# Performance work log

Hardware: AMD Instinct MI355X
Metric: run time of the kernel (lower is better)

The kernel has to match this reference:

```python
import jax, jax.numpy as jnp
import numpy as np

NEG_SLOPE = 0.2

def sage_mean(src_h, dst_h, sidx, didx, n_dst, W_self, W_neigh, bias, edge_weight=None):
    # DGL SAGEConv 'mean': h = fc_self(dst) + fc_neigh(mean_{e in N(v)} src[e] * ew[e]) + bias
    m = src_h[sidx]                                   # [E, d] gather
    if edge_weight is not None:
        m = m * edge_weight[:, None]
    agg = jax.ops.segment_sum(m, didx, num_segments=n_dst)           # [n_dst, d]
    deg = jax.ops.segment_sum(jnp.ones((didx.shape[0],), m.dtype), didx, num_segments=n_dst)
    neigh = agg / jnp.maximum(deg, 1.0)[:, None]      # zero-degree nodes -> 0 (DGL behavior)
    return dst_h @ W_self.T + neigh @ W_neigh.T + bias


def setup_inputs() -> dict:
    key = jax.random.key(0)
    ks = jax.random.split(key, 20)
    n_k, n_e, d, E = 10000, 100000, 128, 1600000
    L = 2
    s = 0.05  # weight scale ~ xavier-ish
    inp = {
        'ii': jax.random.normal(ks[0], (n_k, d), jnp.float32),
        'e_emb': jax.random.normal(ks[1], (n_e, d), jnp.float32),
        'k_emb_weight': jax.random.normal(ks[2], (n_k, d), jnp.float32),
        'cf_ew': jax.random.uniform(ks[3], (E,), jnp.float32),
        'belong_src': jax.random.randint(ks[4], (E,), 0, n_k),
        'belong_dst': jax.random.randint(ks[5], (E,), 0, n_e),
        'collab_src': jax.random.randint(ks[6], (E,), 0, n_e),
        'collab_dst': jax.random.randint(ks[7], (E,), 0, n_e),
        'ek_self': jax.random.normal(ks[8], (L, d, d), jnp.float32) * s,
        'ek_neigh': jax.random.normal(ks[9], (L, d, d), jnp.float32) * s,
        'ek_bias': jnp.zeros((L, d), jnp.float32),
        'ee_self': jax.random.normal(ks[10], (L, d, d), jnp.float32) * s,
        'ee_neigh': jax.random.normal(ks[11], (L, d, d), jnp.float32) * s,
        'ee_bias': jnp.zeros((L, d), jnp.float32),
        'w1_W': jax.random.normal(ks[12], (d, 2 * d), jnp.float32) * s,
        'w1_b': jnp.zeros((d,), jnp.float32),
        'w2_W': jax.random.normal(ks[13], (d, d), jnp.float32) * s,
        'w2_b': jnp.zeros((d,), jnp.float32),
        'w3_W': jax.random.normal(ks[14], (d, d), jnp.float32) * s,
        'w3_b': jnp.zeros((d,), jnp.float32),
        'w4_W': jax.random.normal(ks[15], (d, 2 * d), jnp.float32) * s,
        'w4_b': jnp.zeros((d,), jnp.float32),
        'comb_W': jax.random.normal(ks[16], (d, 2 * d), jnp.float32) * s,
        'comb_b': jnp.zeros((d,), jnp.float32),
    }
    return inp


def reference(ii, e_emb, k_emb_weight, cf_ew, belong_src, belong_dst, collab_src, collab_dst,
              ek_self, ek_neigh, ek_bias, ee_self, ee_neigh, ee_bias,
              w1_W, w1_b, w2_W, w2_b, w3_W, w3_b, w4_W, w4_b, comb_W, comb_b):
    n_e = e_emb.shape[0]
    L = ek_self.shape[0]
    # ii = w4([ii ; k_emb.weight])
    ii2 = jnp.concatenate([ii, k_emb_weight], axis=1) @ w4_W.T + w4_b
    # knowledge -> employee SAGE stack ('belong')
    dst = e_emb
    for i in range(L - 1):
        dst = jax.nn.relu(sage_mean(ii2, dst, belong_src, belong_dst, n_e,
                                    ek_self[i], ek_neigh[i], ek_bias[i]))
    h_iI = sage_mean(ii2, dst, belong_src, belong_dst, n_e,
                     ek_self[L - 1], ek_neigh[L - 1], ek_bias[L - 1])
    h_iI = h_iI @ w2_W.T + w2_b
    # employee -> employee SAGE stack ('collaborate', edge-weighted)
    src_com = jnp.concatenate([h_iI, e_emb], axis=1) @ w1_W.T + w1_b
    dst = e_emb
    for i in range(L - 1):
        dst = jax.nn.relu(sage_mean(src_com, dst, collab_src, collab_dst, n_e,
                                    ee_self[i], ee_neigh[i], ee_bias[i], cf_ew))
    h_iS = sage_mean(src_com, dst, collab_src, collab_dst, n_e,
                     ee_self[L - 1], ee_neigh[L - 1], ee_bias[L - 1], cf_ew)
    h_iS = h_iS @ w3_W.T + w3_b
    h = jnp.concatenate([h_iI, h_iS], axis=1) @ comb_W.T + comb_b
    return jnp.where(h >= 0, h, NEG_SLOPE * h)  # LeakyReLU(0.2)
```

## Files before the change

kernel.cpp:

```cpp
#include <hip/hip_runtime.h>

#define D 128

using f16   = _Float16;
using f16x4 = __attribute__((ext_vector_type(4))) _Float16;
using f16x8 = __attribute__((ext_vector_type(8))) _Float16;
using f32x4 = __attribute__((ext_vector_type(4))) float;

__device__ __forceinline__ f16x8 zero8() {
    f16x8 v;
    #pragma unroll
    for (int j = 0; j < 8; ++j) v[j] = (f16)0;
    return v;
}

template<bool H>
__device__ __forceinline__ void stage_and_mfma(
    const void* Xv, const float* W, int ws,
    f16 (*sX)[136], f16 (*sW)[136],
    int tid, int row0, int M, int wave, int lm, int lg, f32x4 acc[8])
{
    __syncthreads();
    if (H) {
        const f16* X = (const f16*)Xv;
        #pragma unroll
        for (int i = 0; i < 4; ++i) {
            int idx = i * 256 + tid;
            int r   = idx >> 4;
            int kc  = idx & 15;
            f16x8 v = zero8();
            int gr = row0 + r;
            if (gr < M) v = *reinterpret_cast<const f16x8*>(X + (size_t)gr * D + kc * 8);
            *reinterpret_cast<f16x8*>(&sX[r][kc * 8]) = v;
        }
    } else {
        const float* X = (const float*)Xv;
        #pragma unroll
        for (int i = 0; i < 8; ++i) {
            int idx = i * 256 + tid;
            int r   = idx >> 5;
            int kq  = idx & 31;
            float4 v = make_float4(0.f, 0.f, 0.f, 0.f);
            int gr = row0 + r;
            if (gr < M) v = *reinterpret_cast<const float4*>(X + (size_t)gr * D + kq * 4);
            f16x4 h; h[0] = (f16)v.x; h[1] = (f16)v.y; h[2] = (f16)v.z; h[3] = (f16)v.w;
            *reinterpret_cast<f16x4*>(&sX[r][kq * 4]) = h;
        }
    }
    #pragma unroll
    for (int i = 0; i < 16; ++i) {
        int idx = i * 256 + tid;
        int c   = idx >> 5;
        int kq  = idx & 31;
        float4 v = *reinterpret_cast<const float4*>(W + (size_t)c * ws + kq * 4);
        f16x4 h; h[0] = (f16)v.x; h[1] = (f16)v.y; h[2] = (f16)v.z; h[3] = (f16)v.w;
        *reinterpret_cast<f16x4*>(&sW[c][kq * 4]) = h;
    }
    __syncthreads();
    #pragma unroll
    for (int ks = 0; ks < 4; ++ks) {
        f16x8 a = *reinterpret_cast<const f16x8*>(&sX[wave * 16 + lm][ks * 32 + lg * 8]);
        #pragma unroll
        for (int n0 = 0; n0 < 8; ++n0) {
            f16x8 b = *reinterpret_cast<const f16x8*>(&sW[n0 * 16 + lm][ks * 32 + lg * 8]);
            acc[n0] = __builtin_amdgcn_mfma_f32_16x16x32_f16(a, b, acc[n0], 0, 0, 0);
        }
    }
}

template<int ACT, bool X1H, bool X2H, bool O16>
__global__ __launch_bounds__(256, 3)
void gemm_dual_mfma(const void* __restrict__ X1, const float* __restrict__ W1, int ws1,
                    const void* __restrict__ X2, const float* __restrict__ W2, int ws2,
                    const float* __restrict__ bias, void* __restrict__ out, int M)
{
    __shared__ f16 sX[64][136];
    __shared__ f16 sW[128][136];
    const int tid  = threadIdx.x;
    const int row0 = blockIdx.x * 64;
    const int wave = tid >> 6;
    const int lane = tid & 63;
    const int lm   = lane & 15;
    const int lg   = lane >> 4;

    f32x4 acc[8];
    #pragma unroll
    for (int i = 0; i < 8; ++i) acc[i] = (f32x4){0.f, 0.f, 0.f, 0.f};

    stage_and_mfma<X1H>(X1, W1, ws1, sX, sW, tid, row0, M, wave, lm, lg, acc);
    stage_and_mfma<X2H>(X2, W2, ws2, sX, sW, tid, row0, M, wave, lm, lg, acc);

    #pragma unroll
    for (int n0 = 0; n0 < 8; ++n0) {
        int col = n0 * 16 + lm;
        float bv = bias[col];
        #pragma unroll
        for (int r = 0; r < 4; ++r) {
            int row = row0 + wave * 16 + lg * 4 + r;
            if (row < M) {
                float o = acc[n0][r] + bv;
                if (ACT == 1) o = fmaxf(o, 0.f);
                else if (ACT == 2) o = o >= 0.f ? o : 0.2f * o;
                if (O16) ((f16*)out)[(size_t)row * D + col] = (f16)o;
                else     ((float*)out)[(size_t)row * D + col] = o;
            }
        }
    }
}

__global__ void hist_dst(const int* __restrict__ dst, int* __restrict__ cnt, int E)
{
    int e = blockIdx.x * blockDim.x + threadIdx.x;
    if (e < E) atomicAdd(&cnt[dst[e]], 1);
}

__global__ void scan_sums(const int* __restrict__ cnt, int* __restrict__ bsums, int n)
{
    __shared__ int sdata[256];
    int base = blockIdx.x * 1024;
    int t = threadIdx.x;
    int s = 0;
    #pragma unroll
    for (int j = 0; j < 4; ++j) {
        int i = base + t * 4 + j;
        if (i < n) s += cnt[i];
    }
    sdata[t] = s;
    __syncthreads();
    for (int off = 128; off > 0; off >>= 1) {
        if (t < off) sdata[t] += sdata[t + off];
        __syncthreads();
    }
    if (t == 0) bsums[blockIdx.x] = sdata[0];
}

__global__ void scan_bsums(int* __restrict__ bsums, int nb)
{
    if (blockIdx.x == 0 && threadIdx.x == 0) {
        int run = 0;
        for (int i = 0; i < nb; ++i) { int v = bsums[i]; bsums[i] = run; run += v; }
    }
}

__global__ void scan_apply(const int* __restrict__ cnt, const int* __restrict__ bsums,
                           int* __restrict__ rowptr, int* __restrict__ cursor, int n, int E)
{
    __shared__ int sthread[256];
    int base = blockIdx.x * 1024;
    int t = threadIdx.x;
    int vals[4]; int s = 0;
    #pragma unroll
    for (int j = 0; j < 4; ++j) {
        int i = base + t * 4 + j;
        vals[j] = (i < n) ? cnt[i] : 0;
        s += vals[j];
    }
    sthread[t] = s;
    __syncthreads();
    int pre = 0;
    for (int i = 0; i < t; ++i) pre += sthread[i];
    pre += bsums[blockIdx.x];
    #pragma unroll
    for (int j = 0; j < 4; ++j) {
        int i = base + t * 4 + j;
        if (i < n) { rowptr[i] = pre; cursor[i] = pre; pre += vals[j]; }
    }
    if (blockIdx.x == 0 && t == 0) rowptr[n] = E;
}

__global__ void fill_csr(const int* __restrict__ src, const int* __restrict__ dst,
                         const float* __restrict__ ew,
                         int* __restrict__ cursor, int2* __restrict__ epk, int E)
{
    int e = blockIdx.x * blockDim.x + threadIdx.x;
    if (e >= E) return;
    int p = atomicAdd(&cursor[dst[e]], 1);
    float w = ew ? ew[e] : 1.0f;
    epk[p] = make_int2(src[e], __float_as_int(w));
}

__global__ __launch_bounds__(256)
void gather_mean16(const f16* __restrict__ X, const int* __restrict__ rowptr,
                   const int2* __restrict__ epk, f16* __restrict__ agg, int n)
{
    int t = blockIdx.x * blockDim.x + threadIdx.x;
    int node = t >> 6;
    if (node >= n) return;
    int lane = t & 63;
    int h = lane >> 4;
    int q = lane & 15;
    int beg = rowptr[node], end = rowptr[node + 1];
    float acc[8] = {};
    for (int e = beg + h; e < end; e += 4) {
        int2 p = epk[e];
        float w = __int_as_float(p.y);
        f16x8 v = *reinterpret_cast<const f16x8*>(X + (size_t)p.x * D + q * 8);
        #pragma unroll
        for (int j = 0; j < 8; ++j) acc[j] = fmaf((float)v[j], w, acc[j]);
    }
    #pragma unroll
    for (int j = 0; j < 8; ++j) {
        acc[j] += __shfl_xor(acc[j], 16);
        acc[j] += __shfl_xor(acc[j], 32);
    }
    if (h == 0) {
        float inv = 1.0f / fmaxf((float)(end - beg), 1.0f);
        f16x8 o;
        #pragma unroll
        for (int j = 0; j < 8; ++j) o[j] = (f16)(acc[j] * inv);
        *reinterpret_cast<f16x8*>(agg + (size_t)node * D + q * 8) = o;
    }
}

__global__ void fold_weights(const float* __restrict__ w2_W, const float* __restrict__ w2_b,
                             const float* __restrict__ S1, const float* __restrict__ N1,
                             const float* __restrict__ b1,
                             const float* __restrict__ w3_W, const float* __restrict__ w3_b,
                             const float* __restrict__ T1, const float* __restrict__ U1,
                             const float* __restrict__ e1,
                             float* __restrict__ S1f, float* __restrict__ N1f, float* __restrict__ b1f,
                             float* __restrict__ T1f, float* __restrict__ U1f, float* __restrict__ e1f)
{
    int b = blockIdx.x;
    int tid = threadIdx.x;
    if (b < 256) {
        int m = b >> 6;
        const float* WA = (m < 2) ? w2_W : w3_W;
        const float* SB = (m == 0) ? S1 : (m == 1) ? N1 : (m == 2) ? T1 : U1;
        float* O        = (m == 0) ? S1f : (m == 1) ? N1f : (m == 2) ? T1f : U1f;
        int elem = (b & 63) * 256 + tid;
        int i = elem >> 7;
        int k = elem & 127;
        float sum = 0.f;
        for (int j = 0; j < 128; ++j)
            sum = fmaf(WA[i * 128 + j], SB[j * 128 + k], sum);
        O[elem] = sum;
    } else if (b == 256) {
        if (tid < 128) {
            float sum = w2_b[tid];
            for (int j = 0; j < 128; ++j) sum = fmaf(w2_W[tid * 128 + j], b1[j], sum);
            b1f[tid] = sum;
        }
    } else {
        if (tid < 128) {
            float sum = w3_b[tid];
            for (int j = 0; j < 128; ++j) sum = fmaf(w3_W[tid * 128 + j], e1[j], sum);
            e1f[tid] = sum;
        }
    }
}

extern "C" void kernel_launch(void* const* d_in, const int* in_sizes, int n_in,
                              void* d_out, int out_size, void* d_ws, size_t ws_size,
                              hipStream_t stream)
{
    const float* ii      = (const float*)d_in[0];
    const float* e_emb   = (const float*)d_in[1];
    const float* kemb    = (const float*)d_in[2];
    const float* cf_ew   = (const float*)d_in[3];
    const int*   b_src   = (const int*)d_in[4];
    const int*   b_dst   = (const int*)d_in[5];
    const int*   c_src   = (const int*)d_in[6];
    const int*   c_dst   = (const int*)d_in[7];
    const float* ek_self = (const float*)d_in[8];
    const float* ek_neigh= (const float*)d_in[9];
    const float* ek_bias = (const float*)d_in[10];
    const float* ee_self = (const float*)d_in[11];
    const float* ee_neigh= (const float*)d_in[12];
    const float* ee_bias = (const float*)d_in[13];
    const float* w1_W    = (const float*)d_in[14];
    const float* w1_b    = (const float*)d_in[15];
    const float* w2_W    = (const float*)d_in[16];
    const float* w2_b    = (const float*)d_in[17];
    const float* w3_W    = (const float*)d_in[18];
    const float* w3_b    = (const float*)d_in[19];
    const float* w4_W    = (const float*)d_in[20];
    const float* w4_b    = (const float*)d_in[21];
    const float* comb_W  = (const float*)d_in[22];
    const float* comb_b  = (const float*)d_in[23];

    const int n_k = in_sizes[0] / D;
    const int n_e = in_sizes[1] / D;
    const int E   = in_sizes[4];

    char* wsb = (char*)d_ws;
    auto align256 = [](size_t x) { return (x + 255) & ~(size_t)255; };
    const size_t row16 = align256((size_t)n_e * D * sizeof(f16));
    f16*  A16    = (f16*)wsb;   wsb += row16;
    f16*  AGG16  = (f16*)wsb;   wsb += row16;
    f16*  H16    = (f16*)wsb;   wsb += row16;
    f16*  II2    = (f16*)wsb;   wsb += align256((size_t)n_k * D * sizeof(f16));
    int*  rowptr = (int*)wsb;   wsb += align256((size_t)(n_e + 1) * sizeof(int));
    int*  cursor = (int*)wsb;   wsb += align256((size_t)n_e * sizeof(int));
    int2* epk    = (int2*)wsb;  wsb += align256((size_t)E * sizeof(int2));
    int*  bsums  = (int*)wsb;   wsb += 4096;
    float* S1f   = (float*)wsb; wsb += D * D * sizeof(float);
    float* N1f   = (float*)wsb; wsb += D * D * sizeof(float);
    float* T1f   = (float*)wsb; wsb += D * D * sizeof(float);
    float* U1f   = (float*)wsb; wsb += D * D * sizeof(float);
    float* b1f   = (float*)wsb; wsb += 256;
    float* e1f   = (float*)wsb; wsb += 256;
    float* OUT   = (float*)d_out;

    const int gemmGridE = (n_e + 63) / 64;
    const int gemmGridK = (n_k + 63) / 64;
    const int edgeGrid  = (E + 255) / 256;
    const int scanNB    = (n_e + 1023) / 1024;
    const int gathGrid  = (n_e * 64 + 255) / 256;

    fold_weights<<<258, 256, 0, stream>>>(w2_W, w2_b,
        ek_self + D*D, ek_neigh + D*D, ek_bias + D,
        w3_W, w3_b,
        ee_self + D*D, ee_neigh + D*D, ee_bias + D,
        S1f, N1f, b1f, T1f, U1f, e1f);

    gemm_dual_mfma<0, false, false, true><<<gemmGridK, 256, 0, stream>>>(
        ii, w4_W, 2*D, kemb, w4_W + D, 2*D, w4_b, II2, n_k);

    hipMemsetAsync(cursor, 0, (size_t)n_e * sizeof(int), stream);
    hist_dst<<<edgeGrid, 256, 0, stream>>>(b_dst, cursor, E);
    scan_sums<<<scanNB, 256, 0, stream>>>(cursor, bsums, n_e);
    scan_bsums<<<1, 64, 0, stream>>>(bsums, scanNB);
    scan_apply<<<scanNB, 256, 0, stream>>>(cursor, bsums, rowptr, cursor, n_e, E);
    fill_csr<<<edgeGrid, 256, 0, stream>>>(b_src, b_dst, nullptr, cursor, epk, E);
    gather_mean16<<<gathGrid, 256, 0, stream>>>(II2, rowptr, epk, AGG16, n_e);

    gemm_dual_mfma<1, false, true, true><<<gemmGridE, 256, 0, stream>>>(
        e_emb, ek_self, D, AGG16, ek_neigh, D, ek_bias, A16, n_e);

    gemm_dual_mfma<0, true, true, true><<<gemmGridE, 256, 0, stream>>>(
        A16, S1f, D, AGG16, N1f, D, b1f, H16, n_e);

    gemm_dual_mfma<0, true, false, true><<<gemmGridE, 256, 0, stream>>>(
        H16, w1_W, 2*D, e_emb, w1_W + D, 2*D, w1_b, A16, n_e);

    hipMemsetAsync(cursor, 0, (size_t)n_e * sizeof(int), stream);
    hist_dst<<<edgeGrid, 256, 0, stream>>>(c_dst, cursor, E);
    scan_sums<<<scanNB, 256, 0, stream>>>(cursor, bsums, n_e);
    scan_bsums<<<1, 64, 0, stream>>>(bsums, scanNB);
    scan_apply<<<scanNB, 256, 0, stream>>>(cursor, bsums, rowptr, cursor, n_e, E);
    fill_csr<<<edgeGrid, 256, 0, stream>>>(c_src, c_dst, cf_ew, cursor, epk, E);
    gather_mean16<<<gathGrid, 256, 0, stream>>>(A16, rowptr, epk, AGG16, n_e);

    gemm_dual_mfma<1, false, true, true><<<gemmGridE, 256, 0, stream>>>(
        e_emb, ee_self, D, AGG16, ee_neigh, D, ee_bias, A16, n_e);

    gemm_dual_mfma<0, true, true, true><<<gemmGridE, 256, 0, stream>>>(
        A16, T1f, D, AGG16, U1f, D, e1f, A16, n_e);

    gemm_dual_mfma<2, true, true, false><<<gemmGridE, 256, 0, stream>>>(
        H16, comb_W, 2*D, A16, comb_W + D, 2*D, comb_b, OUT, n_e);
}
```

Measured before the change: 874.7 us.

## Fuse chained SAGE layer GEMMs per row tile into single kernels

Replaces the three back-to-back dual GEMM launches on the belong side and the two on the collaborate side with one fused kernel each. Each fused kernel keeps the row tile of e_emb, the aggregated neighbours and the intermediate layer activations in shared memory, so the intermediate A16/H16 round trips through global memory and the repeated e_emb and AGG loads go away. The cost is more shared memory per block (launch bounds drop to two blocks per CU), more serialized weight staging with extra barriers inside one block, and fp16 rounding of intermediates kept in LDS.

```diff
diff --git a/kernel.cpp b/kernel.cpp
--- a/kernel.cpp
+++ b/kernel.cpp
@@ -12,6 +12,201 @@
     #pragma unroll
     for (int j = 0; j < 8; ++j) v[j] = (f16)0;
     return v;
+}
+
+__device__ __forceinline__ void stageX32(const float* __restrict__ X, f16 (*sX)[136],
+                                         int tid, int row0, int M)
+{
+    #pragma unroll
+    for (int i = 0; i < 8; ++i) {
+        int idx = i * 256 + tid;
+        int r = idx >> 5, kq = idx & 31;
+        float4 v = make_float4(0.f, 0.f, 0.f, 0.f);
+        int gr = row0 + r;
+        if (gr < M) v = *reinterpret_cast<const float4*>(X + (size_t)gr * D + kq * 4);
+        f16x4 h; h[0] = (f16)v.x; h[1] = (f16)v.y; h[2] = (f16)v.z; h[3] = (f16)v.w;
+        *reinterpret_cast<f16x4*>(&sX[r][kq * 4]) = h;
+    }
+}
+
+__device__ __forceinline__ void stageX16(const f16* __restrict__ X, f16 (*sX)[136],
+                                         int tid, int row0, int M)
+{
+    #pragma unroll
+    for (int i = 0; i < 4; ++i) {
+        int idx = i * 256 + tid;
+        int r = idx >> 4, kc = idx & 15;
+        f16x8 v = zero8();
+        int gr = row0 + r;
+        if (gr < M) v = *reinterpret_cast<const f16x8*>(X + (size_t)gr * D + kc * 8);
+        *reinterpret_cast<f16x8*>(&sX[r][kc * 8]) = v;
+    }
+}
+
+__device__ __forceinline__ void stageW(const float* __restrict__ W, int ws,
+                                       f16 (*sW)[136], int tid)
+{
+    #pragma unroll
+    for (int i = 0; i < 16; ++i) {
+        int idx = i * 256 + tid;
+        int c = idx >> 5, kq = idx & 31;
+        float4 v = *reinterpret_cast<const float4*>(W + (size_t)c * ws + kq * 4);
+        f16x4 h; h[0] = (f16)v.x; h[1] = (f16)v.y; h[2] = (f16)v.z; h[3] = (f16)v.w;
+        *reinterpret_cast<f16x4*>(&sW[c][kq * 4]) = h;
+    }
+}
+
+__device__ __forceinline__ void mfma8(const f16 (*sA)[136], const f16 (*sW)[136],
+                                      int wave, int lm, int lg, f32x4 acc[8])
+{
+    #pragma unroll
+    for (int ks = 0; ks < 4; ++ks) {
+        f16x8 a = *reinterpret_cast<const f16x8*>(&sA[wave * 16 + lm][ks * 32 + lg * 8]);
+        #pragma unroll
+        for (int n0 = 0; n0 < 8; ++n0) {
+            f16x8 b = *reinterpret_cast<const f16x8*>(&sW[n0 * 16 + lm][ks * 32 + lg * 8]);
+            acc[n0] = __builtin_amdgcn_mfma_f32_16x16x32_f16(a, b, acc[n0], 0, 0, 0);
+        }
+    }
+}
+
+__global__ __launch_bounds__(256, 2)
+void fused_ek(const float* __restrict__ e_emb, const f16* __restrict__ agg,
+              const float* __restrict__ S0, const float* __restrict__ N0,
+              const float* __restrict__ b0,
+              const float* __restrict__ S1f, const float* __restrict__ N1f,
+              const float* __restrict__ b1f,
+              const float* __restrict__ w1W, const float* __restrict__ w1b,
+              f16* __restrict__ H16, f16* __restrict__ A16, int M)
+{
+    __shared__ f16 sE[64][136];
+    __shared__ f16 sG[64][136];
+    __shared__ f16 sW[128][136];
+    const int tid = threadIdx.x, row0 = blockIdx.x * 64;
+    const int wave = tid >> 6, lane = tid & 63, lm = lane & 15, lg = lane >> 4;
+
+    f32x4 acc1[8], acc2[8];
+    #pragma unroll
+    for (int i = 0; i < 8; ++i) { acc1[i] = (f32x4){0,0,0,0}; acc2[i] = (f32x4){0,0,0,0}; }
+
+    stageX32(e_emb, sE, tid, row0, M);
+    stageW(S0, D, sW, tid);
+    __syncthreads();
+    mfma8(sE, sW, wave, lm, lg, acc1);
+    __syncthreads();
+    stageW(w1W + D, 2 * D, sW, tid);
+    __syncthreads();
+    mfma8(sE, sW, wave, lm, lg, acc2);
+    __syncthreads();
+    stageX16(agg, sG, tid, row0, M);
+    stageW(N0, D, sW, tid);
+    __syncthreads();
+    mfma8(sG, sW, wave, lm, lg, acc1);
+    #pragma unroll
+    for (int n0 = 0; n0 < 8; ++n0) {
+        int col = n0 * 16 + lm;
+        float bv = b0[col];
+        #pragma unroll
+        for (int r = 0; r < 4; ++r) {
+            float v = fmaxf(acc1[n0][r] + bv, 0.f);
+            sE[wave * 16 + lg * 4 + r][col] = (f16)v;
+        }
+    }
+    __syncthreads();
+    stageW(S1f, D, sW, tid);
+    __syncthreads();
+    #pragma unroll
+    for (int i = 0; i < 8; ++i) acc1[i] = (f32x4){0,0,0,0};
+    mfma8(sE, sW, wave, lm, lg, acc1);
+    __syncthreads();
+    stageW(N1f, D, sW, tid);
+    __syncthreads();
+    mfma8(sG, sW, wave, lm, lg, acc1);
+    #pragma unroll
+    for (int n0 = 0; n0 < 8; ++n0) {
+        int col = n0 * 16 + lm;
+        float bv = b1f[col];
+        #pragma unroll
+        for (int r = 0; r < 4; ++r) {
+            int row = row0 + wave * 16 + lg * 4 + r;
+            float v = acc1[n0][r] + bv;
+            sE[wave * 16 + lg * 4 + r][col] = (f16)v;
+            if (row < M) H16[(size_t)row * D + col] = (f16)v;
+        }
+    }
+    __syncthreads();
+    stageW(w1W, 2 * D, sW, tid);
+    __syncthreads();
+    mfma8(sE, sW, wave, lm, lg, acc2);
+    #pragma unroll
+    for (int n0 = 0; n0 < 8; ++n0) {
+        int col = n0 * 16 + lm;
+        float bv = w1b[col];
+        #pragma unroll
+        for (int r = 0; r < 4; ++r) {
+            int row = row0 + wave * 16 + lg * 4 + r;
+            if (row < M) A16[(size_t)row * D + col] = (f16)(acc2[n0][r] + bv);
+        }
+    }
+}
+
+__global__ __launch_bounds__(256, 2)
+void fused_ee(const float* __restrict__ e_emb, const f16* __restrict__ agg,
+              const float* __restrict__ T0, const float* __restrict__ U0,
+              const float* __restrict__ eb0,
+              const float* __restrict__ T1f, const float* __restrict__ U1f,
+              const float* __restrict__ e1f,
+              f16* __restrict__ A16, int M)
+{
+    __shared__ f16 sE[64][136];
+    __shared__ f16 sG[64][136];
+    __shared__ f16 sW[128][136];
+    const int tid = threadIdx.x, row0 = blockIdx.x * 64;
+    const int wave = tid >> 6, lane = tid & 63, lm = lane & 15, lg = lane >> 4;
+
+    f32x4 acc1[8];
+    #pragma unroll
+    for (int i = 0; i < 8; ++i) acc1[i] = (f32x4){0,0,0,0};
+
+    stageX32(e_emb, sE, tid, row0, M);
+    stageW(T0, D, sW, tid);
+    __syncthreads();
+    mfma8(sE, sW, wave, lm, lg, acc1);
+    __syncthreads();
+    stageX16(agg, sG, tid, row0, M);
+    stageW(U0, D, sW, tid);
+    __syncthreads();
+    mfma8(sG, sW, wave, lm, lg, acc1);
+    #pragma unroll
+    for (int n0 = 0; n0 < 8; ++n0) {
+        int col = n0 * 16 + lm;
+        float bv = eb0[col];
+        #pragma unroll
+        for (int r = 0; r < 4; ++r) {
+            float v = fmaxf(acc1[n0][r] + bv, 0.f);
+            sE[wave * 16 + lg * 4 + r][col] = (f16)v;
+        }
+    }
+    __syncthreads();
+    stageW(T1f, D, sW, tid);
+    __syncthreads();
+    #pragma unroll
+    for (int i = 0; i < 8; ++i) acc1[i] = (f32x4){0,0,0,0};
+    mfma8(sE, sW, wave, lm, lg, acc1);
+    __syncthreads();
+    stageW(U1f, D, sW, tid);
+    __syncthreads();
+    mfma8(sG, sW, wave, lm, lg, acc1);
+    #pragma unroll
+    for (int n0 = 0; n0 < 8; ++n0) {
+        int col = n0 * 16 + lm;
+        float bv = e1f[col];
+        #pragma unroll
+        for (int r = 0; r < 4; ++r) {
+            int row = row0 + wave * 16 + lg * 4 + r;
+            if (row < M) A16[(size_t)row * D + col] = (f16)(acc1[n0][r] + bv);
+        }
+    }
 }
 
 template<bool H>
@@ -21,51 +216,11 @@
     int tid, int row0, int M, int wave, int lm, int lg, f32x4 acc[8])
 {
     __syncthreads();
-    if (H) {
-        const f16* X = (const f16*)Xv;
-        #pragma unroll
-        for (int i = 0; i < 4; ++i) {
-            int idx = i * 256 + tid;
-            int r   = idx >> 4;
-            int kc  = idx & 15;
-            f16x8 v = zero8();
-            int gr = row0 + r;
-            if (gr < M) v = *reinterpret_cast<const f16x8*>(X + (size_t)gr * D + kc * 8);
-            *reinterpret_cast<f16x8*>(&sX[r][kc * 8]) = v;
-        }
-    } else {
-        const float* X = (const float*)Xv;
-        #pragma unroll
-        for (int i = 0; i < 8; ++i) {
-            int idx = i * 256 + tid;
-            int r   = idx >> 5;
-            int kq  = idx & 31;
-            float4 v = make_float4(0.f, 0.f, 0.f, 0.f);
-            int gr = row0 + r;
-            if (gr < M) v = *reinterpret_cast<const float4*>(X + (size_t)gr * D + kq * 4);
-            f16x4 h; h[0] = (f16)v.x; h[1] = (f16)v.y; h[2] = (f16)v.z; h[3] = (f16)v.w;
-            *reinterpret_cast<f16x4*>(&sX[r][kq * 4]) = h;
-        }
-    }
-    #pragma unroll
-    for (int i = 0; i < 16; ++i) {
-        int idx = i * 256 + tid;
-        int c   = idx >> 5;
-        int kq  = idx & 31;
-        float4 v = *reinterpret_cast<const float4*>(W + (size_t)c * ws + kq * 4);
-        f16x4 h; h[0] = (f16)v.x; h[1] = (f16)v.y; h[2] = (f16)v.z; h[3] = (f16)v.w;
-        *reinterpret_cast<f16x4*>(&sW[c][kq * 4]) = h;
-    }
-    __syncthreads();
-    #pragma unroll
-    for (int ks = 0; ks < 4; ++ks) {
-        f16x8 a = *reinterpret_cast<const f16x8*>(&sX[wave * 16 + lm][ks * 32 + lg * 8]);
-        #pragma unroll
-        for (int n0 = 0; n0 < 8; ++n0) {
-            f16x8 b = *reinterpret_cast<const f16x8*>(&sW[n0 * 16 + lm][ks * 32 + lg * 8]);
-            acc[n0] = __builtin_amdgcn_mfma_f32_16x16x32_f16(a, b, acc[n0], 0, 0, 0);
-        }
-    }
+    if (H) stageX16((const f16*)Xv, sX, tid, row0, M);
+    else   stageX32((const float*)Xv, sX, tid, row0, M);
+    stageW(W, ws, sW, tid);
+    __syncthreads();
+    mfma8(sX, sW, wave, lm, lg, acc);
 }
 
 template<int ACT, bool X1H, bool X2H, bool O16>
@@ -76,16 +231,12 @@
 {
     __shared__ f16 sX[64][136];
     __shared__ f16 sW[128][136];
-    const int tid  = threadIdx.x;
-    const int row0 = blockIdx.x * 64;
-    const int wave = tid >> 6;
-    const int lane = tid & 63;
-    const int lm   = lane & 15;
-    const int lg   = lane >> 4;
+    const int tid = threadIdx.x, row0 = blockIdx.x * 64;
+    const int wave = tid >> 6, lane = tid & 63, lm = lane & 15, lg = lane >> 4;
 
     f32x4 acc[8];
     #pragma unroll
-    for (int i = 0; i < 8; ++i) acc[i] = (f32x4){0.f, 0.f, 0.f, 0.f};
+    for (int i = 0; i < 8; ++i) acc[i] = (f32x4){0,0,0,0};
 
     stage_and_mfma<X1H>(X1, W1, ws1, sX, sW, tid, row0, M, wave, lm, lg, acc);
     stage_and_mfma<X2H>(X2, W2, ws2, sX, sW, tid, row0, M, wave, lm, lg, acc);
@@ -325,14 +476,9 @@
     fill_csr<<<edgeGrid, 256, 0, stream>>>(b_src, b_dst, nullptr, cursor, epk, E);
     gather_mean16<<<gathGrid, 256, 0, stream>>>(II2, rowptr, epk, AGG16, n_e);
 
-    gemm_dual_mfma<1, false, true, true><<<gemmGridE, 256, 0, stream>>>(
-        e_emb, ek_self, D, AGG16, ek_neigh, D, ek_bias, A16, n_e);
-
-    gemm_dual_mfma<0, true, true, true><<<gemmGridE, 256, 0, stream>>>(
-        A16, S1f, D, AGG16, N1f, D, b1f, H16, n_e);
-
-    gemm_dual_mfma<0, true, false, true><<<gemmGridE, 256, 0, stream>>>(
-        H16, w1_W, 2*D, e_emb, w1_W + D, 2*D, w1_b, A16, n_e);
+    fused_ek<<<gemmGridE, 256, 0, stream>>>(
+        e_emb, AGG16, ek_self, ek_neigh, ek_bias,
+        S1f, N1f, b1f, w1_W, w1_b, H16, A16, n_e);
 
     hipMemsetAsync(cursor, 0, (size_t)n_e * sizeof(int), stream);
     hist_dst<<<edgeGrid, 256, 0, stream>>>(c_dst, cursor, E);
@@ -342,11 +488,9 @@
     fill_csr<<<edgeGrid, 256, 0, stream>>>(c_src, c_dst, cf_ew, cursor, epk, E);
     gather_mean16<<<gathGrid, 256, 0, stream>>>(A16, rowptr, epk, AGG16, n_e);
 
-    gemm_dual_mfma<1, false, true, true><<<gemmGridE, 256, 0, stream>>>(
-        e_emb, ee_self, D, AGG16, ee_neigh, D, ee_bias, A16, n_e);
-
-    gemm_dual_mfma<0, true, true, true><<<gemmGridE, 256, 0, stream>>>(
-        A16, T1f, D, AGG16, U1f, D, e1f, A16, n_e);
+    fused_ee<<<gemmGridE, 256, 0, stream>>>(
+        e_emb, AGG16, ee_self, ee_neigh, ee_bias,
+        T1f, U1f, e1f, A16, n_e);
 
     gemm_dual_mfma<2, true, true, false><<<gemmGridE, 256, 0, stream>>>(
         H16, comb_W, 2*D, A16, comb_W + D, 2*D, comb_b, OUT, n_e);
```

Result: faster. 805.6 us (-7.9%).
